# Performance work log

Hardware: AMD Instinct MI355X
Metric: run time of the kernel (lower is better)

Reference implementation:

```python
import jax, jax.numpy as jnp
import numpy as np

UNITS, B, I, H = 8, 65536, 256, 256


def setup_inputs() -> dict:
    key = jax.random.key(0)
    k_x, k_wi, k_wh, k_bi, k_bh = jax.random.split(key, 5)
    scale = 1.0 / np.sqrt(H)  # torch GRUCell init range ~ U(-1/sqrt(H), 1/sqrt(H))
    return {
        "x": jax.random.normal(k_x, (B, I), dtype=jnp.float32),
        "W_ih": jax.random.uniform(k_wi, (UNITS, 3 * H, I), jnp.float32, -scale, scale),
        "W_hh": jax.random.uniform(k_wh, (UNITS, 3 * H, H), jnp.float32, -scale, scale),
        "b_ih": jax.random.uniform(k_bi, (UNITS, 3 * H), jnp.float32, -scale, scale),
        "b_hh": jax.random.uniform(k_bh, (UNITS, 3 * H), jnp.float32, -scale, scale),
        "h0": jnp.zeros((H,), dtype=jnp.float32),
    }


def _gru_chain(x, W_ih, W_hh, b_ih, b_hh, h0):
    # h starts as h0 broadcast over batch; each of the `units` cells consumes
    # the SAME x and the previous cell's output as hidden state.
    h_init = jnp.broadcast_to(h0, (x.shape[0], h0.shape[0]))

    def step(h, params):
        Wih, Whh, bih, bhh = params
        gi = x @ Wih.T + bih            # [B, 3H] input gates
        gh = h @ Whh.T + bhh            # [B, 3H] hidden gates
        i_r, i_z, i_n = jnp.split(gi, 3, axis=-1)  # torch gate order: r, z, n
        h_r, h_z, h_n = jnp.split(gh, 3, axis=-1)
        r = jax.nn.sigmoid(i_r + h_r)
        z = jax.nn.sigmoid(i_z + h_z)
        n = jnp.tanh(i_n + r * h_n)
        h_new = (1.0 - z) * n + z * h
        return h_new, None

    h_final, _ = jax.lax.scan(step, h_init, (W_ih, W_hh, b_ih, b_hh))
    return h_final


def reference(x, W_ih, W_hh, b_ih, b_hh, h0):
    return _gru_chain(x, W_ih, W_hh, b_ih, b_hh, h0)
```

## Files before the change

### kernel.cpp

```cpp
#include <hip/hip_runtime.h>
#include <hip/hip_bf16.h>

typedef __bf16 bf16;
typedef __bf16 bf16x4 __attribute__((ext_vector_type(4)));
typedef __bf16 bf16x8 __attribute__((ext_vector_type(8)));
typedef float f32x4 __attribute__((ext_vector_type(4)));

#define GLD16(gp, sp) __builtin_amdgcn_global_load_lds( \
    (const __attribute__((address_space(1))) void*)(gp), \
    (__attribute__((address_space(3))) void*)(sp), 16, 0, 0)

#define FENCE() asm volatile("" ::: "memory")
#define BARRIER() do { FENCE(); __builtin_amdgcn_s_barrier(); FENCE(); } while (0)

constexpr int UNITS = 8;
constexpr int BATCH = 65536;
constexpr int DIM   = 256;
constexpr int BM    = 256;
constexpr int BN    = 16;
constexpr int BK    = 64;
constexpr int JT    = DIM / BN;
constexpr int PAIRS = DIM / BK;
constexpr int STEPS_PER_UNIT = JT * PAIRS;
constexpr int TOT_STEPS = UNITS * STEPS_PER_UNIT;
constexpr int WTILE = 3 * BN * BK;
constexpr size_t WN = (size_t)UNITS * 3 * DIM * DIM;

__device__ __forceinline__ float sigmoidf_fast(float x) {
    return 1.0f / (1.0f + __expf(-x));
}
__device__ __forceinline__ float tanhf_fast(float x) {
    float y = fminf(fmaxf(x, -15.0f), 15.0f);
    float e = __expf(-2.0f * y);
    return (1.0f - e) / (1.0f + e);
}
__device__ __forceinline__ unsigned hsoff(int row, int col) {
    return (unsigned)((row * DIM + col) * 2) ^ (unsigned)((row & 7) << 4);
}
__device__ __forceinline__ float bfbits2f(unsigned b) {
    return __builtin_bit_cast(float, b << 16);
}
__device__ __forceinline__ unsigned f2bfbits(float f) {
    return (unsigned)__builtin_bit_cast(unsigned short, (bf16)f);
}

__global__ void convert_kernel(const float* __restrict__ Wih,
                               const float* __restrict__ Whh,
                               const float* __restrict__ bih,
                               const float* __restrict__ bhh,
                               bf16* __restrict__ Wihbf,
                               bf16* __restrict__ Whhbf,
                               float* __restrict__ bcomb)
{
    const size_t W4 = 2 * WN / 4;
    size_t i = (size_t)blockIdx.x * blockDim.x + threadIdx.x;
    if (i < W4) {
        size_t e = i * 4;
        const float* src = (e < WN) ? Wih : Whh;
        bf16* dst        = (e < WN) ? Wihbf : Whhbf;
        size_t off       = (e < WN) ? e : e - WN;
        const float4 v = *(const float4*)(src + off);
        bf16x4 o;
        o[0] = (bf16)v.x; o[1] = (bf16)v.y; o[2] = (bf16)v.z; o[3] = (bf16)v.w;
        *(bf16x4*)(dst + off) = o;
    } else {
        size_t j = i - W4;
        if (j < (size_t)UNITS * 1024) {
            int u = (int)(j >> 10), t = (int)(j & 1023);
            const float* bi = bih + u * 768;
            const float* bh = bhh + u * 768;
            float v;
            if (t < 512)      v = bi[t] + bh[t];
            else if (t < 768) v = bi[t];
            else              v = bh[t - 256];
            bcomb[u * 1024 + t] = v;
        }
    }
}

__device__ __forceinline__ void stage_w(const bf16* __restrict__ Wihbf,
                                        const bf16* __restrict__ Whhbf,
                                        bf16* wb, int sg, int wave, int lane)
{
    const int u    = sg >> 6;
    const int jt   = (sg >> 2) & 15;
    const int pair = sg & 3;
    const int k0   = pair * 64;
    const bf16* Wi = Wihbf + (size_t)u * (3 * DIM * DIM);
    const bf16* Wh = Whhbf + (size_t)u * (3 * DIM * DIM);
    const int rr   = lane >> 3;
    const int scol = ((lane & 7) ^ rr) << 3;
    {
        const int c  = wave;
        const bf16* W = (c < 6) ? Wi : Wh;
        const int cc = (c < 6) ? c : c - 6;
        bf16* d = wb + ((c < 6) ? 0 : WTILE) + cc * 512;
        const int r = cc * 8 + rr;
        const int grow = (r >> 4) * DIM + jt * BN + (r & 15);
        GLD16(W + (size_t)grow * DIM + k0 + scol, d);
    }
    if (wave < 4) {
        const int cc = wave + 2;
        const int r = cc * 8 + rr;
        const int grow = (r >> 4) * DIM + jt * BN + (r & 15);
        GLD16(Wh + (size_t)grow * DIM + k0 + scol, wb + WTILE + cc * 512);
    }
}

#define READ6(BI, BH, WT, KC2) do {                                          \
    _Pragma("unroll")                                                        \
    for (int g_ = 0; g_ < 3; ++g_) {                                         \
        const int off_ = (g_ * BN + l15) * BK                                \
                       + ((((KC2) * 4 + quad) ^ (l15 & 7)) << 3);            \
        BI[g_] = *(const bf16x8*)((WT) + off_);                              \
        BH[g_] = *(const bf16x8*)((WT) + WTILE + off_);                      \
    }                                                                        \
} while (0)

#define MFMA12(BI, BH, KCG) do {                                             \
    __builtin_amdgcn_s_setprio(1);                                           \
    _Pragma("unroll")                                                        \
    for (int mt_ = 0; mt_ < 2; ++mt_) {                                      \
        acc[0][mt_] = __builtin_amdgcn_mfma_f32_16x16x32_bf16(xf[mt_][KCG], BI[0], acc[0][mt_], 0, 0, 0); \
        acc[0][mt_] = __builtin_amdgcn_mfma_f32_16x16x32_bf16(hf[mt_][KCG], BH[0], acc[0][mt_], 0, 0, 0); \
        acc[1][mt_] = __builtin_amdgcn_mfma_f32_16x16x32_bf16(xf[mt_][KCG], BI[1], acc[1][mt_], 0, 0, 0); \
        acc[1][mt_] = __builtin_amdgcn_mfma_f32_16x16x32_bf16(hf[mt_][KCG], BH[1], acc[1][mt_], 0, 0, 0); \
        acc[2][mt_] = __builtin_amdgcn_mfma_f32_16x16x32_bf16(xf[mt_][KCG], BI[2], acc[2][mt_], 0, 0, 0); \
        acc[3][mt_] = __builtin_amdgcn_mfma_f32_16x16x32_bf16(hf[mt_][KCG], BH[2], acc[3][mt_], 0, 0, 0); \
    }                                                                        \
    __builtin_amdgcn_s_setprio(0);                                           \
} while (0)

__global__ __launch_bounds__(512, 2)
void gru_fused_kernel(const float* __restrict__ xg,
                      const float* __restrict__ h0g,
                      const bf16* __restrict__ Wihbf,
                      const bf16* __restrict__ Whhbf,
                      const float* __restrict__ bcomb,
                      float* __restrict__ out)
{
    __shared__ __align__(16) bf16 hs[BM * DIM];
    __shared__ __align__(16) bf16 wbuf[2][2 * WTILE];

    const int tid  = threadIdx.x;
    const int wave = tid >> 6;
    const int lane = tid & 63;
    const int quad = lane >> 4;
    const int l15  = lane & 15;
    const int odd  = l15 & 1;
    const int m0   = blockIdx.x * BM;

    bf16x8 xf[2][8];
#pragma unroll
    for (int mt = 0; mt < 2; ++mt) {
        const int row = m0 + wave * 32 + mt * 16 + l15;
        const float* xr = xg + (size_t)row * DIM + quad * 8;
#pragma unroll
        for (int kc = 0; kc < 8; ++kc) {
            const float4 a = *(const float4*)(xr + kc * 32);
            const float4 b = *(const float4*)(xr + kc * 32 + 4);
            bf16x8 v;
            v[0]=(bf16)a.x; v[1]=(bf16)a.y; v[2]=(bf16)a.z; v[3]=(bf16)a.w;
            v[4]=(bf16)b.x; v[5]=(bf16)b.y; v[6]=(bf16)b.z; v[7]=(bf16)b.w;
            xf[mt][kc] = v;
        }
    }

    bf16x8 hf[2][8];
#pragma unroll
    for (int kc = 0; kc < 8; ++kc) {
        const float4 a = *(const float4*)(h0g + kc * 32 + quad * 8);
        const float4 b = *(const float4*)(h0g + kc * 32 + quad * 8 + 4);
        bf16x8 v;
        v[0]=(bf16)a.x; v[1]=(bf16)a.y; v[2]=(bf16)a.z; v[3]=(bf16)a.w;
        v[4]=(bf16)b.x; v[5]=(bf16)b.y; v[6]=(bf16)b.z; v[7]=(bf16)b.w;
        hf[0][kc] = v;
        hf[1][kc] = v;
    }
#pragma unroll
    for (int mt = 0; mt < 2; ++mt)
#pragma unroll
        for (int kc = 0; kc < 8; ++kc)
            *(bf16x8*)((char*)hs + hsoff(wave * 32 + mt * 16 + l15,
                                         kc * 32 + quad * 8)) = hf[mt][kc];

    float bc0, bc1, bc2, bc3;
    float bn0 = 0.f, bn1 = 0.f, bn2 = 0.f, bn3 = 0.f;
    {
        const float* bp = bcomb + l15;
        bc0 = bp[0]; bc1 = bp[256]; bc2 = bp[512]; bc3 = bp[768];
    }
    stage_w(Wihbf, Whhbf, (bf16*)wbuf[0], 0, wave, lane);

    for (int u = 0; u < UNITS; ++u) {
        for (int jt = 0; jt < JT; ++jt) {
            f32x4 acc[4][2];
#pragma unroll
            for (int mt = 0; mt < 2; ++mt) {
                acc[0][mt] = (f32x4){bc0, bc0, bc0, bc0};
                acc[1][mt] = (f32x4){bc1, bc1, bc1, bc1};
                acc[2][mt] = (f32x4){bc2, bc2, bc2, bc2};
                acc[3][mt] = (f32x4){bc3, bc3, bc3, bc3};
            }
            bf16x8 biA[3], bhA[3], biB[3], bhB[3];
            const int sgb = u * STEPS_PER_UNIT + jt * PAIRS;

#pragma unroll
            for (int pair = 0; pair < PAIRS; ++pair) {
                if (pair == 1) MFMA12(biB, bhB, 1);
                if (pair == 2) MFMA12(biB, bhB, 3);
                if (pair == 3) MFMA12(biB, bhB, 5);

                asm volatile("s_waitcnt vmcnt(0)" ::: "memory");
                BARRIER();
                const bf16* wt = wbuf[pair & 1];
                READ6(biA, bhA, wt, 0);
                if (sgb + pair + 1 < TOT_STEPS)
                    stage_w(Wihbf, Whhbf, (bf16*)wbuf[(pair + 1) & 1],
                            sgb + pair + 1, wave, lane);
                if (pair == 1) {
                    const int njt = (jt + 1) & 15;
                    const int nu  = (jt == 15) ? u + 1 : u;
                    if (nu < UNITS) {
                        const float* bp = bcomb + nu * 1024 + njt * BN + l15;
                        bn0 = bp[0]; bn1 = bp[256]; bn2 = bp[512]; bn3 = bp[768];
                    }
                }
                if (pair == 0) MFMA12(biA, bhA, 0);
                if (pair == 1) MFMA12(biA, bhA, 2);
                if (pair == 2) MFMA12(biA, bhA, 4);
                if (pair == 3) MFMA12(biA, bhA, 6);
                READ6(biB, bhB, wt, 1);
            }
            MFMA12(biB, bhB, 7);

#pragma unroll
            for (int mt = 0; mt < 2; ++mt) {
                const int rbase = wave * 32 + mt * 16 + quad * 4;
                const int rowA  = rbase + 2 * odd;
                const int colb  = jt * BN + (l15 & ~1);
                const unsigned d0 = *(const unsigned*)((const char*)hs + hsoff(rowA,     colb));
                const unsigned d1 = *(const unsigned*)((const char*)hs + hsoff(rowA + 1, colb));
                const unsigned o0 = (unsigned)__shfl_xor((int)d0, 1);
                const unsigned o1 = (unsigned)__shfl_xor((int)d1, 1);
                const unsigned p0 = odd ? o0 : d0;
                const unsigned p1 = odd ? o1 : d1;
                const unsigned p2 = odd ? d0 : o0;
                const unsigned p3 = odd ? d1 : o1;
                const int sh = odd ? 16 : 0;
                float hp[4];
                hp[0] = bfbits2f((p0 >> sh) & 0xffffu);
                hp[1] = bfbits2f((p1 >> sh) & 0xffffu);
                hp[2] = bfbits2f((p2 >> sh) & 0xffffu);
                hp[3] = bfbits2f((p3 >> sh) & 0xffffu);
                unsigned bb[4];
#pragma unroll
                for (int i = 0; i < 4; ++i) {
                    const float r_ = sigmoidf_fast(acc[0][mt][i]);
                    const float z_ = sigmoidf_fast(acc[1][mt][i]);
                    const float n_ = tanhf_fast(acc[2][mt][i] + r_ * acc[3][mt][i]);
                    const float hv = fmaf(z_, hp[i] - n_, n_);
                    bb[i] = f2bfbits(hv);
                }
                const unsigned lo  = bb[0] | (bb[1] << 16);
                const unsigned hi  = bb[2] | (bb[3] << 16);
                const unsigned olo = (unsigned)__shfl_xor((int)lo, 1);
                const unsigned ohi = (unsigned)__shfl_xor((int)hi, 1);
                unsigned w0, w1;
                if (odd) {
                    w0 = (ohi & 0xffffu) | (hi << 16);
                    w1 = (ohi >> 16)     | (hi & 0xffff0000u);
                } else {
                    w0 = (lo & 0xffffu)  | (olo << 16);
                    w1 = (lo >> 16)      | (olo & 0xffff0000u);
                }
                *(unsigned*)((char*)hs + hsoff(rowA,     colb)) = w0;
                *(unsigned*)((char*)hs + hsoff(rowA + 1, colb)) = w1;
            }
            bc0 = bn0; bc1 = bn1; bc2 = bn2; bc3 = bn3;
        }
        if (u < UNITS - 1) {
#pragma unroll
            for (int mt = 0; mt < 2; ++mt)
#pragma unroll
                for (int kc = 0; kc < 8; ++kc)
                    hf[mt][kc] = *(const bf16x8*)((const char*)hs +
                        hsoff(wave * 32 + mt * 16 + l15, kc * 32 + quad * 8));
        }
    }

    __syncthreads();
    {
        const int c8 = (tid & 31) * 8;
        const int r0 = tid >> 5;
#pragma unroll
        for (int i = 0; i < 16; ++i) {
            const int r = r0 + i * 16;
            const bf16x8 v = *(const bf16x8*)((const char*)hs + hsoff(r, c8));
            float4 a, b;
            a.x = (float)v[0]; a.y = (float)v[1]; a.z = (float)v[2]; a.w = (float)v[3];
            b.x = (float)v[4]; b.y = (float)v[5]; b.z = (float)v[6]; b.w = (float)v[7];
            float* o = out + (size_t)(m0 + r) * DIM + c8;
            *(float4*)o       = a;
            *(float4*)(o + 4) = b;
        }
    }
}

extern "C" void kernel_launch(void* const* d_in, const int* in_sizes, int n_in,
                              void* d_out, int out_size, void* d_ws, size_t ws_size,
                              hipStream_t stream) {
    const float* x   = (const float*)d_in[0];
    const float* Wih = (const float*)d_in[1];
    const float* Whh = (const float*)d_in[2];
    const float* bih = (const float*)d_in[3];
    const float* bhh = (const float*)d_in[4];
    const float* h0  = (const float*)d_in[5];
    float* out = (float*)d_out;

    bf16* Wihbf  = (bf16*)d_ws;
    bf16* Whhbf  = Wihbf + WN;
    float* bcomb = (float*)(Whhbf + WN);

    {
        const size_t total = 2 * WN / 4 + (size_t)UNITS * 1024;
        const int cblocks = (int)((total + 255) / 256);
        hipLaunchKernelGGL(convert_kernel, dim3(cblocks), dim3(256), 0, stream,
                           Wih, Whh, bih, bhh, Wihbf, Whhbf, bcomb);
    }
    hipLaunchKernelGGL(gru_fused_kernel, dim3(BATCH / BM), dim3(512), 0, stream,
                       x, h0, Wihbf, Whhbf, bcomb, out);
}
```

Baseline: 700.8 us.

## Prepack weights into MFMA fragment order and load directly into registers

The convert kernel now packs the bf16 weights in the exact per-lane MFMA B-fragment order, so each wave reads its 6 fragments per k-chunk with one contiguous 16-byte global load per lane. The LDS weight double buffer, global_load_lds staging, and per-pair vmcnt waits and barriers are removed in favour of a two-deep register prefetch, leaving one barrier per column tile. This cuts synchronisation and LDS traffic and frees LDS. In exchange, every wave issues its own global/L2 loads for the same weights, and load latency is hidden only by one chunk of MFMA work.

```diff
diff --git a/kernel.cpp b/kernel.cpp
--- a/kernel.cpp
+++ b/kernel.cpp
@@ -5,10 +5,6 @@
 typedef __bf16 bf16x4 __attribute__((ext_vector_type(4)));
 typedef __bf16 bf16x8 __attribute__((ext_vector_type(8)));
 typedef float f32x4 __attribute__((ext_vector_type(4)));
-
-#define GLD16(gp, sp) __builtin_amdgcn_global_load_lds( \
-    (const __attribute__((address_space(1))) void*)(gp), \
-    (__attribute__((address_space(3))) void*)(sp), 16, 0, 0)
 
 #define FENCE() asm volatile("" ::: "memory")
 #define BARRIER() do { FENCE(); __builtin_amdgcn_s_barrier(); FENCE(); } while (0)
@@ -18,12 +14,10 @@
 constexpr int DIM   = 256;
 constexpr int BM    = 256;
 constexpr int BN    = 16;
-constexpr int BK    = 64;
 constexpr int JT    = DIM / BN;
-constexpr int PAIRS = DIM / BK;
-constexpr int STEPS_PER_UNIT = JT * PAIRS;
-constexpr int TOT_STEPS = UNITS * STEPS_PER_UNIT;
-constexpr int WTILE = 3 * BN * BK;
+constexpr int KC    = 8;
+constexpr int TOTSS = UNITS * JT * KC;
+constexpr int CHUNK = 6 * 64 * 8;
 constexpr size_t WN = (size_t)UNITS * 3 * DIM * DIM;
 
 __device__ __forceinline__ float sigmoidf_fast(float x) {
@@ -48,23 +42,30 @@
                                const float* __restrict__ Whh,
                                const float* __restrict__ bih,
                                const float* __restrict__ bhh,
-                               bf16* __restrict__ Wihbf,
-                               bf16* __restrict__ Whhbf,
+                               bf16* __restrict__ Wpk,
                                float* __restrict__ bcomb)
 {
-    const size_t W4 = 2 * WN / 4;
+    const size_t W8 = 2 * WN / 8;
     size_t i = (size_t)blockIdx.x * blockDim.x + threadIdx.x;
-    if (i < W4) {
-        size_t e = i * 4;
-        const float* src = (e < WN) ? Wih : Whh;
-        bf16* dst        = (e < WN) ? Wihbf : Whhbf;
-        size_t off       = (e < WN) ? e : e - WN;
-        const float4 v = *(const float4*)(src + off);
-        bf16x4 o;
-        o[0] = (bf16)v.x; o[1] = (bf16)v.y; o[2] = (bf16)v.z; o[3] = (bf16)v.w;
-        *(bf16x4*)(dst + off) = o;
+    if (i < W8) {
+        const int ss   = (int)(i / 384);
+        const int r    = (int)(i % 384);
+        const int gi   = r >> 6;
+        const int lane = r & 63;
+        const int kc = ss & 7, jt = (ss >> 3) & 15, u = ss >> 7;
+        const int g  = (gi < 3) ? gi : gi - 3;
+        const float* W = ((gi < 3) ? Wih : Whh) + (size_t)u * 3 * DIM * DIM;
+        const int row = g * DIM + jt * BN + (lane & 15);
+        const int col = kc * 32 + (lane >> 4) * 8;
+        const float* s = W + (size_t)row * DIM + col;
+        const float4 a = *(const float4*)(s);
+        const float4 b = *(const float4*)(s + 4);
+        bf16x8 v;
+        v[0]=(bf16)a.x; v[1]=(bf16)a.y; v[2]=(bf16)a.z; v[3]=(bf16)a.w;
+        v[4]=(bf16)b.x; v[5]=(bf16)b.y; v[6]=(bf16)b.z; v[7]=(bf16)b.w;
+        *(bf16x8*)(Wpk + i * 8) = v;
     } else {
-        size_t j = i - W4;
+        size_t j = i - W8;
         if (j < (size_t)UNITS * 1024) {
             int u = (int)(j >> 10), t = (int)(j & 1023);
             const float* bi = bih + u * 768;
@@ -78,55 +79,23 @@
     }
 }
 
-__device__ __forceinline__ void stage_w(const bf16* __restrict__ Wihbf,
-                                        const bf16* __restrict__ Whhbf,
-                                        bf16* wb, int sg, int wave, int lane)
-{
-    const int u    = sg >> 6;
-    const int jt   = (sg >> 2) & 15;
-    const int pair = sg & 3;
-    const int k0   = pair * 64;
-    const bf16* Wi = Wihbf + (size_t)u * (3 * DIM * DIM);
-    const bf16* Wh = Whhbf + (size_t)u * (3 * DIM * DIM);
-    const int rr   = lane >> 3;
-    const int scol = ((lane & 7) ^ rr) << 3;
-    {
-        const int c  = wave;
-        const bf16* W = (c < 6) ? Wi : Wh;
-        const int cc = (c < 6) ? c : c - 6;
-        bf16* d = wb + ((c < 6) ? 0 : WTILE) + cc * 512;
-        const int r = cc * 8 + rr;
-        const int grow = (r >> 4) * DIM + jt * BN + (r & 15);
-        GLD16(W + (size_t)grow * DIM + k0 + scol, d);
-    }
-    if (wave < 4) {
-        const int cc = wave + 2;
-        const int r = cc * 8 + rr;
-        const int grow = (r >> 4) * DIM + jt * BN + (r & 15);
-        GLD16(Wh + (size_t)grow * DIM + k0 + scol, wb + WTILE + cc * 512);
-    }
-}
-
-#define READ6(BI, BH, WT, KC2) do {                                          \
+#define LOADW(B6, SS) do {                                                   \
+    const bf16* p_ = wl + (size_t)(SS) * CHUNK;                              \
     _Pragma("unroll")                                                        \
-    for (int g_ = 0; g_ < 3; ++g_) {                                         \
-        const int off_ = (g_ * BN + l15) * BK                                \
-                       + ((((KC2) * 4 + quad) ^ (l15 & 7)) << 3);            \
-        BI[g_] = *(const bf16x8*)((WT) + off_);                              \
-        BH[g_] = *(const bf16x8*)((WT) + WTILE + off_);                      \
-    }                                                                        \
+    for (int gi_ = 0; gi_ < 6; ++gi_)                                        \
+        B6[gi_] = *(const bf16x8*)(p_ + gi_ * 512);                          \
 } while (0)
 
-#define MFMA12(BI, BH, KCG) do {                                             \
+#define MFMA12(B6, KCG) do {                                                 \
     __builtin_amdgcn_s_setprio(1);                                           \
     _Pragma("unroll")                                                        \
     for (int mt_ = 0; mt_ < 2; ++mt_) {                                      \
-        acc[0][mt_] = __builtin_amdgcn_mfma_f32_16x16x32_bf16(xf[mt_][KCG], BI[0], acc[0][mt_], 0, 0, 0); \
-        acc[0][mt_] = __builtin_amdgcn_mfma_f32_16x16x32_bf16(hf[mt_][KCG], BH[0], acc[0][mt_], 0, 0, 0); \
-        acc[1][mt_] = __builtin_amdgcn_mfma_f32_16x16x32_bf16(xf[mt_][KCG], BI[1], acc[1][mt_], 0, 0, 0); \
-        acc[1][mt_] = __builtin_amdgcn_mfma_f32_16x16x32_bf16(hf[mt_][KCG], BH[1], acc[1][mt_], 0, 0, 0); \
-        acc[2][mt_] = __builtin_amdgcn_mfma_f32_16x16x32_bf16(xf[mt_][KCG], BI[2], acc[2][mt_], 0, 0, 0); \
-        acc[3][mt_] = __builtin_amdgcn_mfma_f32_16x16x32_bf16(hf[mt_][KCG], BH[2], acc[3][mt_], 0, 0, 0); \
+        acc[0][mt_] = __builtin_amdgcn_mfma_f32_16x16x32_bf16(xf[mt_][KCG], B6[0], acc[0][mt_], 0, 0, 0); \
+        acc[0][mt_] = __builtin_amdgcn_mfma_f32_16x16x32_bf16(hf[mt_][KCG], B6[3], acc[0][mt_], 0, 0, 0); \
+        acc[1][mt_] = __builtin_amdgcn_mfma_f32_16x16x32_bf16(xf[mt_][KCG], B6[1], acc[1][mt_], 0, 0, 0); \
+        acc[1][mt_] = __builtin_amdgcn_mfma_f32_16x16x32_bf16(hf[mt_][KCG], B6[4], acc[1][mt_], 0, 0, 0); \
+        acc[2][mt_] = __builtin_amdgcn_mfma_f32_16x16x32_bf16(xf[mt_][KCG], B6[2], acc[2][mt_], 0, 0, 0); \
+        acc[3][mt_] = __builtin_amdgcn_mfma_f32_16x16x32_bf16(hf[mt_][KCG], B6[5], acc[3][mt_], 0, 0, 0); \
     }                                                                        \
     __builtin_amdgcn_s_setprio(0);                                           \
 } while (0)
@@ -134,13 +103,11 @@
 __global__ __launch_bounds__(512, 2)
 void gru_fused_kernel(const float* __restrict__ xg,
                       const float* __restrict__ h0g,
-                      const bf16* __restrict__ Wihbf,
-                      const bf16* __restrict__ Whhbf,
+                      const bf16* __restrict__ Wpk,
                       const float* __restrict__ bcomb,
                       float* __restrict__ out)
 {
     __shared__ __align__(16) bf16 hs[BM * DIM];
-    __shared__ __align__(16) bf16 wbuf[2][2 * WTILE];
 
     const int tid  = threadIdx.x;
     const int wave = tid >> 6;
@@ -190,10 +157,16 @@
         const float* bp = bcomb + l15;
         bc0 = bp[0]; bc1 = bp[256]; bc2 = bp[512]; bc3 = bp[768];
     }
-    stage_w(Wihbf, Whhbf, (bf16*)wbuf[0], 0, wave, lane);
+
+    const bf16* wl = Wpk + (size_t)lane * 8;
+    bf16x8 bw[2][6];
+    LOADW(bw[0], 0);
+    LOADW(bw[1], 1);
 
     for (int u = 0; u < UNITS; ++u) {
         for (int jt = 0; jt < JT; ++jt) {
+            BARRIER();
+
             f32x4 acc[4][2];
 #pragma unroll
             for (int mt = 0; mt < 2; ++mt) {
@@ -202,37 +175,22 @@
                 acc[2][mt] = (f32x4){bc2, bc2, bc2, bc2};
                 acc[3][mt] = (f32x4){bc3, bc3, bc3, bc3};
             }
-            bf16x8 biA[3], bhA[3], biB[3], bhB[3];
-            const int sgb = u * STEPS_PER_UNIT + jt * PAIRS;
-
-#pragma unroll
-            for (int pair = 0; pair < PAIRS; ++pair) {
-                if (pair == 1) MFMA12(biB, bhB, 1);
-                if (pair == 2) MFMA12(biB, bhB, 3);
-                if (pair == 3) MFMA12(biB, bhB, 5);
-
-                asm volatile("s_waitcnt vmcnt(0)" ::: "memory");
-                BARRIER();
-                const bf16* wt = wbuf[pair & 1];
-                READ6(biA, bhA, wt, 0);
-                if (sgb + pair + 1 < TOT_STEPS)
-                    stage_w(Wihbf, Whhbf, (bf16*)wbuf[(pair + 1) & 1],
-                            sgb + pair + 1, wave, lane);
-                if (pair == 1) {
+            const int sgb = (u * JT + jt) * KC;
+
+#pragma unroll
+            for (int kc = 0; kc < KC; ++kc) {
+                MFMA12(bw[kc & 1], kc);
+                if (sgb + kc + 2 < TOTSS)
+                    LOADW(bw[kc & 1], sgb + kc + 2);
+                if (kc == 1) {
                     const int njt = (jt + 1) & 15;
-                    const int nu  = (jt == 15) ? u + 1 : u;
+                    const int nu  = (jt == JT - 1) ? u + 1 : u;
                     if (nu < UNITS) {
                         const float* bp = bcomb + nu * 1024 + njt * BN + l15;
                         bn0 = bp[0]; bn1 = bp[256]; bn2 = bp[512]; bn3 = bp[768];
                     }
                 }
-                if (pair == 0) MFMA12(biA, bhA, 0);
-                if (pair == 1) MFMA12(biA, bhA, 2);
-                if (pair == 2) MFMA12(biA, bhA, 4);
-                if (pair == 3) MFMA12(biA, bhA, 6);
-                READ6(biB, bhB, wt, 1);
             }
-            MFMA12(biB, bhB, 7);
 
 #pragma unroll
             for (int mt = 0; mt < 2; ++mt) {
@@ -318,16 +276,15 @@
     const float* h0  = (const float*)d_in[5];
     float* out = (float*)d_out;
 
-    bf16* Wihbf  = (bf16*)d_ws;
-    bf16* Whhbf  = Wihbf + WN;
-    float* bcomb = (float*)(Whhbf + WN);
+    bf16* Wpk    = (bf16*)d_ws;
+    float* bcomb = (float*)(Wpk + 2 * WN);
 
     {
-        const size_t total = 2 * WN / 4 + (size_t)UNITS * 1024;
+        const size_t total = 2 * WN / 8 + (size_t)UNITS * 1024;
         const int cblocks = (int)((total + 255) / 256);
         hipLaunchKernelGGL(convert_kernel, dim3(cblocks), dim3(256), 0, stream,
-                           Wih, Whh, bih, bhh, Wihbf, Whhbf, bcomb);
+                           Wih, Whh, bih, bhh, Wpk, bcomb);
     }
     hipLaunchKernelGGL(gru_fused_kernel, dim3(BATCH / BM), dim3(512), 0, stream,
-                       x, h0, Wihbf, Whhbf, bcomb, out);
-}
+                       x, h0, Wpk, bcomb, out);
+}
```

Result: slower. 725.5 us (+3.5%).
